# Optimization experiments

Hardware: AMD Instinct MI355X
Metric: run time of the kernel (lower is better)

Reference implementation:

```python
import jax, jax.numpy as jnp
import numpy as np

B, C, H, W = 4, 64, 64, 64


def setup_inputs() -> dict:
    key = jax.random.key(0)
    k1, k2, k3, k4, k5 = jax.random.split(key, 5)
    return {
        "x": jax.random.normal(k1, (B, C, H, W), dtype=jnp.float32),
        "w_qkv": jax.random.normal(k2, (3 * C, C), dtype=jnp.float32) * (1.0 / np.sqrt(C)),
        "b_qkv": jax.random.normal(k3, (3 * C,), dtype=jnp.float32) * 0.02,
        "w_proj": jax.random.normal(k4, (C, C), dtype=jnp.float32) * (1.0 / np.sqrt(C)),
        "b_proj": jax.random.normal(k5, (C,), dtype=jnp.float32) * 0.02,
    }


def reference(x, w_qkv, b_qkv, w_proj, b_proj):
    b, c, h, w = x.shape
    xf = x.reshape(b, c, h * w)                                  # [B, C, N]
    # 1x1 Conv1d == per-position linear over channels
    qkv = jnp.einsum('oc,bcn->bon', w_qkv, xf) + b_qkv[None, :, None]  # [B, 3C, N]
    q, k, v = jnp.split(qkv, 3, axis=1)                          # each [B, C, N]
    scores = jnp.einsum('bcn,bcm->bnm', q, k) / (c ** 0.5)       # [B, N, N]
    attn = jax.nn.softmax(scores, axis=-1)
    out = jnp.einsum('bcm,bnm->bcn', v, attn)                    # [B, C, N]
    out = jnp.einsum('oc,bcn->bon', w_proj, out) + b_proj[None, :, None]
    return out.reshape(b, c, h, w) + x
```

## Files before the change

### kernel.cpp

```cpp
#include <hip/hip_runtime.h>

typedef __bf16 bf16x8 __attribute__((ext_vector_type(8)));
typedef __bf16 bf16x4 __attribute__((ext_vector_type(4)));
typedef __bf16 bf16x2 __attribute__((ext_vector_type(2)));
typedef float f32x4 __attribute__((ext_vector_type(4)));
typedef short s16x4 __attribute__((ext_vector_type(4)));

#define NB 4
#define NC 64
#define NN 4096
#define SPLIT 8

#define QSCALE (0.125f * 1.44269504088896340736f)

#if __has_builtin(__builtin_amdgcn_exp2f)
#define EXP2(x) __builtin_amdgcn_exp2f(x)
#else
#define EXP2(x) exp2f(x)
#endif

__global__ __launch_bounds__(256) void qkv_kernel(
    const float* __restrict__ x, const float* __restrict__ wqkv,
    const float* __restrict__ bqkv,
    __bf16* __restrict__ Qg, __bf16* __restrict__ Kg, __bf16* __restrict__ Vg)
{
  const int tid = threadIdx.x;
  const int b = blockIdx.y;
  const int z = blockIdx.z;
  const int tsel = z >> 3;
  const int obase = (z & 7) * 8;
  const int n = blockIdx.x * 512 + tid * 2;
  const float wscale = (tsel == 0) ? QSCALE : 1.0f;

  __shared__ float wsh[8 * 64];
  __shared__ float bsh[8];
  wsh[tid]       = wqkv[(tsel * 64 + obase) * 64 + tid] * wscale;
  wsh[tid + 256] = wqkv[(tsel * 64 + obase) * 64 + tid + 256] * wscale;
  if (tid < 8) bsh[tid] = bqkv[tsel * 64 + obase + tid] * wscale;
  __syncthreads();

  float xa[64], xb[64];
#pragma unroll
  for (int c = 0; c < 64; c++) {
    const float2 t = *(const float2*)&x[((size_t)(b * 64 + c)) * NN + n];
    xa[c] = t.x; xb[c] = t.y;
  }

  float aa[8], ab[8];
#pragma unroll
  for (int j = 0; j < 8; j++) { aa[j] = bsh[j]; ab[j] = bsh[j]; }
#pragma unroll
  for (int c4 = 0; c4 < 64; c4 += 4) {
#pragma unroll
    for (int j = 0; j < 8; j++) {
      const float4 wv = *(const float4*)&wsh[j * 64 + c4];
      aa[j] = fmaf(wv.x, xa[c4 + 0], aa[j]);
      aa[j] = fmaf(wv.y, xa[c4 + 1], aa[j]);
      aa[j] = fmaf(wv.z, xa[c4 + 2], aa[j]);
      aa[j] = fmaf(wv.w, xa[c4 + 3], aa[j]);
      ab[j] = fmaf(wv.x, xb[c4 + 0], ab[j]);
      ab[j] = fmaf(wv.y, xb[c4 + 1], ab[j]);
      ab[j] = fmaf(wv.z, xb[c4 + 2], ab[j]);
      ab[j] = fmaf(wv.w, xb[c4 + 3], ab[j]);
    }
  }

  if (tsel == 2) {
#pragma unroll
    for (int j = 0; j < 8; j++) {
      bf16x2 pv;
      pv[0] = (__bf16)aa[j]; pv[1] = (__bf16)ab[j];
      *(bf16x2*)(Vg + ((size_t)(b * 64 + obase + j)) * NN + n) = pv;
    }
  } else {
    __bf16* base = (tsel == 0 ? Qg : Kg);
    bf16x8 p0, p1;
#pragma unroll
    for (int j = 0; j < 8; j++) { p0[j] = (__bf16)aa[j]; p1[j] = (__bf16)ab[j]; }
    *(bf16x8*)(base + ((size_t)(b * NN + n)) * 64 + obase) = p0;
    *(bf16x8*)(base + ((size_t)(b * NN + n + 1)) * 64 + obase) = p1;
  }
}

__global__ __launch_bounds__(256) void flash_kernel(
    const __bf16* __restrict__ Q, const __bf16* __restrict__ K,
    const __bf16* __restrict__ V, __bf16* __restrict__ Opart,
    float* __restrict__ lpart)
{
  const int b = blockIdx.y;
  const int s = blockIdx.z;
  const int tid = threadIdx.x;
  const int wave = tid >> 6;
  const int lane = tid & 63;
  const int quad = lane >> 4;
  const int l16 = lane & 15;

  __shared__ __bf16 Kt[64 * 72];
  __shared__ __bf16 Vt[64 * 72];

  const int q0 = blockIdx.x * 128 + wave * 32;

  bf16x8 qf[2][2];
#pragma unroll
  for (int qt = 0; qt < 2; qt++) {
    const __bf16* qrow = Q + ((size_t)(b * NN + q0 + qt * 16 + l16)) * 64;
    qf[qt][0] = *(const bf16x8*)(qrow + quad * 8);
    qf[qt][1] = *(const bf16x8*)(qrow + 32 + quad * 8);
  }

  f32x4 acc[2][4];
#pragma unroll
  for (int qt = 0; qt < 2; qt++)
#pragma unroll
    for (int ct = 0; ct < 4; ct++) acc[qt][ct] = (f32x4){0.f, 0.f, 0.f, 0.f};
  float l[2] = {0.f, 0.f};

  const int kbeg = s * (NN / SPLIT);
  const int kend = kbeg + (NN / SPLIT);
#pragma unroll 1
  for (int kt0 = kbeg; kt0 < kend; kt0 += 64) {
    __syncthreads();
#pragma unroll
    for (int it = 0; it < 2; it++) {
      const int chunk = tid + it * 256;
      const int row = chunk >> 3, col8 = (chunk & 7) * 8;
      *(bf16x8*)(&Kt[row * 72 + col8]) =
          *(const bf16x8*)(K + ((size_t)(b * NN + kt0 + row)) * 64 + col8);
      *(bf16x8*)(&Vt[row * 72 + col8]) =
          *(const bf16x8*)(V + ((size_t)(b * 64 + row)) * NN + kt0 + col8);
    }
    __syncthreads();

    s16x4 pk[4][2];
#pragma unroll
    for (int t = 0; t < 4; t++) {
      const bf16x8 kf0 = *(const bf16x8*)(&Kt[(t * 16 + l16) * 72 + quad * 8]);
      const bf16x8 kf1 = *(const bf16x8*)(&Kt[(t * 16 + l16) * 72 + 32 + quad * 8]);
#pragma unroll
      for (int qt = 0; qt < 2; qt++) {
        f32x4 z = (f32x4){0.f, 0.f, 0.f, 0.f};
        z = __builtin_amdgcn_mfma_f32_16x16x32_bf16(kf0, qf[qt][0], z, 0, 0, 0);
        z = __builtin_amdgcn_mfma_f32_16x16x32_bf16(kf1, qf[qt][1], z, 0, 0, 0);
        const float p0 = EXP2(z[0]), p1 = EXP2(z[1]);
        const float p2 = EXP2(z[2]), p3 = EXP2(z[3]);
        l[qt] += (p0 + p1) + (p2 + p3);
        bf16x4 pv;
        pv[0] = (__bf16)p0; pv[1] = (__bf16)p1;
        pv[2] = (__bf16)p2; pv[3] = (__bf16)p3;
        pk[t][qt] = __builtin_bit_cast(s16x4, pv);
      }
    }

#pragma unroll
    for (int kg = 0; kg < 4; kg++) {
#pragma unroll
      for (int ct = 0; ct < 4; ct++) {
        const bf16x4 va =
            *(const bf16x4*)(&Vt[(ct * 16 + l16) * 72 + kg * 16 + quad * 4]);
        const s16x4 a = __builtin_bit_cast(s16x4, va);
        acc[0][ct] = __builtin_amdgcn_mfma_f32_16x16x16bf16_1k(
            a, pk[kg][0], acc[0][ct], 0, 0, 0);
        acc[1][ct] = __builtin_amdgcn_mfma_f32_16x16x16bf16_1k(
            a, pk[kg][1], acc[1][ct], 0, 0, 0);
      }
    }
  }

#pragma unroll
  for (int qt = 0; qt < 2; qt++) {
    float lr = l[qt];
    lr += __shfl_xor(lr, 16);
    lr += __shfl_xor(lr, 32);
    if (quad == 0)
      lpart[((size_t)(s * NB + b)) * NN + q0 + qt * 16 + l16] = lr;
#pragma unroll
    for (int ct = 0; ct < 4; ct++)
#pragma unroll
      for (int r = 0; r < 4; r++)
        Opart[(((size_t)(s * NB + b)) * 64 + ct * 16 + quad * 4 + r) * NN +
              q0 + qt * 16 + l16] = (__bf16)acc[qt][ct][r];
  }
}

__global__ __launch_bounds__(256) void combine_proj_kernel(
    const __bf16* __restrict__ Opart, const float* __restrict__ lpart,
    const float* __restrict__ wproj, const float* __restrict__ bproj,
    const float* __restrict__ x, float* __restrict__ out)
{
  const int b = blockIdx.y;
  const int n0 = blockIdx.x * 32;
  const int tid = threadIdx.x;

  __shared__ float Ot[64 * 36];
  __shared__ float wT[64 * 66];
  __shared__ float lsh[32];
  __shared__ float bsh[64];

  if (tid < 32) {
    float lt = 0.f;
#pragma unroll
    for (int s = 0; s < SPLIT; s++)
      lt += lpart[((size_t)(s * NB + b)) * NN + n0 + tid];
    lsh[tid] = 1.0f / lt;
  }
  if (tid < 64) bsh[tid] = bproj[tid];
#pragma unroll
  for (int k = 0; k < 16; k++) {
    const int i = tid + k * 256;
    wT[(i & 63) * 66 + (i >> 6)] = wproj[i];
  }
  __syncthreads();

  {
    const int c = tid >> 2;
    const int n8 = (tid & 3) * 8;
    float o[8];
#pragma unroll
    for (int j = 0; j < 8; j++) o[j] = 0.f;
#pragma unroll
    for (int s = 0; s < SPLIT; s++) {
      const bf16x8 v = *(const bf16x8*)(
          Opart + (((size_t)(s * NB + b)) * 64 + c) * NN + n0 + n8);
#pragma unroll
      for (int j = 0; j < 8; j++) o[j] += (float)v[j];
    }
#pragma unroll
    for (int j = 0; j < 8; j++) Ot[c * 36 + n8 + j] = o[j] * lsh[n8 + j];
  }
  __syncthreads();

  const int co = (tid >> 3) * 2;
  const int ng = (tid & 7) * 4;
  float a0[4], a1[4];
#pragma unroll
  for (int j = 0; j < 4; j++) { a0[j] = bsh[co]; a1[j] = bsh[co + 1]; }
  for (int cin = 0; cin < 64; cin++) {
    const float4 ov = *(const float4*)&Ot[cin * 36 + ng];
    const float2 wv = *(const float2*)&wT[cin * 66 + co];
    a0[0] = fmaf(wv.x, ov.x, a0[0]); a0[1] = fmaf(wv.x, ov.y, a0[1]);
    a0[2] = fmaf(wv.x, ov.z, a0[2]); a0[3] = fmaf(wv.x, ov.w, a0[3]);
    a1[0] = fmaf(wv.y, ov.x, a1[0]); a1[1] = fmaf(wv.y, ov.y, a1[1]);
    a1[2] = fmaf(wv.y, ov.z, a1[2]); a1[3] = fmaf(wv.y, ov.w, a1[3]);
  }

#pragma unroll
  for (int i = 0; i < 2; i++) {
    float* ai = (i == 0) ? a0 : a1;
    const size_t base = ((size_t)(b * 64 + co + i)) * NN + n0 + ng;
    const float4 xr = *(const float4*)&x[base];
    float4 r;
    r.x = ai[0] + xr.x; r.y = ai[1] + xr.y;
    r.z = ai[2] + xr.z; r.w = ai[3] + xr.w;
    *(float4*)&out[base] = r;
  }
}

extern "C" void kernel_launch(void* const* d_in, const int* in_sizes, int n_in,
                              void* d_out, int out_size, void* d_ws, size_t ws_size,
                              hipStream_t stream) {
  const float* x     = (const float*)d_in[0];
  const float* wqkv  = (const float*)d_in[1];
  const float* bqkv  = (const float*)d_in[2];
  const float* wproj = (const float*)d_in[3];
  const float* bproj = (const float*)d_in[4];
  float* out = (float*)d_out;

  char* ws = (char*)d_ws;
  __bf16* Q     = (__bf16*)(ws);
  __bf16* K     = (__bf16*)(ws + (2u << 20));
  __bf16* V     = (__bf16*)(ws + (4u << 20));
  __bf16* Opart = (__bf16*)(ws + (6u << 20));
  float*  lpart = (float*)(ws + (23u << 20));

  qkv_kernel<<<dim3(8, NB, 24), 256, 0, stream>>>(x, wqkv, bqkv, Q, K, V);
  flash_kernel<<<dim3(32, NB, SPLIT), 256, 0, stream>>>(Q, K, V, Opart, lpart);
  combine_proj_kernel<<<dim3(128, NB), 256, 0, stream>>>(Opart, lpart, wproj,
                                                         bproj, x, out);
}
```

Before: 113.7 us.

## Fuse output projection into flash kernel via MFMA before split combine

```diff
diff --git a/kernel.cpp b/kernel.cpp
--- a/kernel.cpp
+++ b/kernel.cpp
@@ -84,8 +84,8 @@
 
 __global__ __launch_bounds__(256) void flash_kernel(
     const __bf16* __restrict__ Q, const __bf16* __restrict__ K,
-    const __bf16* __restrict__ V, __bf16* __restrict__ Opart,
-    float* __restrict__ lpart)
+    const __bf16* __restrict__ V, const float* __restrict__ wproj,
+    __bf16* __restrict__ Opart, float* __restrict__ lpart)
 {
   const int b = blockIdx.y;
   const int s = blockIdx.z;
@@ -173,86 +173,90 @@
     lr += __shfl_xor(lr, 32);
     if (quad == 0)
       lpart[((size_t)(s * NB + b)) * NN + q0 + qt * 16 + l16] = lr;
-#pragma unroll
-    for (int ct = 0; ct < 4; ct++)
+  }
+
+  s16x4 ob[2][4];
+#pragma unroll
+  for (int qt = 0; qt < 2; qt++)
+#pragma unroll
+    for (int ch = 0; ch < 4; ch++) {
+      bf16x4 t;
+#pragma unroll
+      for (int r = 0; r < 4; r++) t[r] = (__bf16)acc[qt][ch][r];
+      ob[qt][ch] = __builtin_bit_cast(s16x4, t);
+    }
+
+#pragma unroll
+  for (int cot = 0; cot < 4; cot++) {
+    f32x4 po[2];
+    po[0] = (f32x4){0.f, 0.f, 0.f, 0.f};
+    po[1] = (f32x4){0.f, 0.f, 0.f, 0.f};
+#pragma unroll
+    for (int ch = 0; ch < 4; ch++) {
+      const float4 wv =
+          *(const float4*)&wproj[(cot * 16 + l16) * 64 + ch * 16 + quad * 4];
+      bf16x4 wb;
+      wb[0] = (__bf16)wv.x; wb[1] = (__bf16)wv.y;
+      wb[2] = (__bf16)wv.z; wb[3] = (__bf16)wv.w;
+      const s16x4 a = __builtin_bit_cast(s16x4, wb);
+      po[0] = __builtin_amdgcn_mfma_f32_16x16x16bf16_1k(a, ob[0][ch], po[0], 0, 0, 0);
+      po[1] = __builtin_amdgcn_mfma_f32_16x16x16bf16_1k(a, ob[1][ch], po[1], 0, 0, 0);
+    }
+#pragma unroll
+    for (int qt = 0; qt < 2; qt++)
 #pragma unroll
       for (int r = 0; r < 4; r++)
-        Opart[(((size_t)(s * NB + b)) * 64 + ct * 16 + quad * 4 + r) * NN +
-              q0 + qt * 16 + l16] = (__bf16)acc[qt][ct][r];
-  }
-}
-
-__global__ __launch_bounds__(256) void combine_proj_kernel(
+        Opart[(((size_t)(s * NB + b)) * 64 + cot * 16 + quad * 4 + r) * NN +
+              q0 + qt * 16 + l16] = (__bf16)po[qt][r];
+  }
+}
+
+__global__ __launch_bounds__(256) void combine_kernel(
     const __bf16* __restrict__ Opart, const float* __restrict__ lpart,
-    const float* __restrict__ wproj, const float* __restrict__ bproj,
-    const float* __restrict__ x, float* __restrict__ out)
+    const float* __restrict__ bproj, const float* __restrict__ x,
+    float* __restrict__ out)
 {
   const int b = blockIdx.y;
   const int n0 = blockIdx.x * 32;
   const int tid = threadIdx.x;
 
-  __shared__ float Ot[64 * 36];
-  __shared__ float wT[64 * 66];
-  __shared__ float lsh[32];
-  __shared__ float bsh[64];
-
+  __shared__ float linv[32];
   if (tid < 32) {
     float lt = 0.f;
 #pragma unroll
     for (int s = 0; s < SPLIT; s++)
       lt += lpart[((size_t)(s * NB + b)) * NN + n0 + tid];
-    lsh[tid] = 1.0f / lt;
-  }
-  if (tid < 64) bsh[tid] = bproj[tid];
-#pragma unroll
-  for (int k = 0; k < 16; k++) {
-    const int i = tid + k * 256;
-    wT[(i & 63) * 66 + (i >> 6)] = wproj[i];
+    linv[tid] = 1.0f / lt;
   }
   __syncthreads();
 
-  {
-    const int c = tid >> 2;
-    const int n8 = (tid & 3) * 8;
-    float o[8];
-#pragma unroll
-    for (int j = 0; j < 8; j++) o[j] = 0.f;
-#pragma unroll
-    for (int s = 0; s < SPLIT; s++) {
-      const bf16x8 v = *(const bf16x8*)(
-          Opart + (((size_t)(s * NB + b)) * 64 + c) * NN + n0 + n8);
-#pragma unroll
-      for (int j = 0; j < 8; j++) o[j] += (float)v[j];
-    }
-#pragma unroll
-    for (int j = 0; j < 8; j++) Ot[c * 36 + n8 + j] = o[j] * lsh[n8 + j];
-  }
-  __syncthreads();
-
-  const int co = (tid >> 3) * 2;
-  const int ng = (tid & 7) * 4;
-  float a0[4], a1[4];
-#pragma unroll
-  for (int j = 0; j < 4; j++) { a0[j] = bsh[co]; a1[j] = bsh[co + 1]; }
-  for (int cin = 0; cin < 64; cin++) {
-    const float4 ov = *(const float4*)&Ot[cin * 36 + ng];
-    const float2 wv = *(const float2*)&wT[cin * 66 + co];
-    a0[0] = fmaf(wv.x, ov.x, a0[0]); a0[1] = fmaf(wv.x, ov.y, a0[1]);
-    a0[2] = fmaf(wv.x, ov.z, a0[2]); a0[3] = fmaf(wv.x, ov.w, a0[3]);
-    a1[0] = fmaf(wv.y, ov.x, a1[0]); a1[1] = fmaf(wv.y, ov.y, a1[1]);
-    a1[2] = fmaf(wv.y, ov.z, a1[2]); a1[3] = fmaf(wv.y, ov.w, a1[3]);
-  }
-
-#pragma unroll
-  for (int i = 0; i < 2; i++) {
-    float* ai = (i == 0) ? a0 : a1;
-    const size_t base = ((size_t)(b * 64 + co + i)) * NN + n0 + ng;
-    const float4 xr = *(const float4*)&x[base];
-    float4 r;
-    r.x = ai[0] + xr.x; r.y = ai[1] + xr.y;
-    r.z = ai[2] + xr.z; r.w = ai[3] + xr.w;
-    *(float4*)&out[base] = r;
-  }
+  const int c = tid >> 2;
+  const int n8 = (tid & 3) * 8;
+
+  float o[8];
+#pragma unroll
+  for (int j = 0; j < 8; j++) o[j] = 0.f;
+#pragma unroll
+  for (int s = 0; s < SPLIT; s++) {
+    const bf16x8 v = *(const bf16x8*)(
+        Opart + (((size_t)(s * NB + b)) * 64 + c) * NN + n0 + n8);
+#pragma unroll
+    for (int j = 0; j < 8; j++) o[j] += (float)v[j];
+  }
+
+  const float bb = bproj[c];
+  const float4 li0 = *(const float4*)&linv[n8];
+  const float4 li1 = *(const float4*)&linv[n8 + 4];
+  const size_t base = ((size_t)(b * 64 + c)) * NN + n0 + n8;
+  const float4 x0 = *(const float4*)&x[base];
+  const float4 x1 = *(const float4*)&x[base + 4];
+  float4 r0, r1;
+  r0.x = o[0] * li0.x + bb + x0.x;  r0.y = o[1] * li0.y + bb + x0.y;
+  r0.z = o[2] * li0.z + bb + x0.z;  r0.w = o[3] * li0.w + bb + x0.w;
+  r1.x = o[4] * li1.x + bb + x1.x;  r1.y = o[5] * li1.y + bb + x1.y;
+  r1.z = o[6] * li1.z + bb + x1.z;  r1.w = o[7] * li1.w + bb + x1.w;
+  *(float4*)&out[base] = r0;
+  *(float4*)&out[base + 4] = r1;
 }
 
 extern "C" void kernel_launch(void* const* d_in, const int* in_sizes, int n_in,
@@ -273,7 +277,8 @@
   float*  lpart = (float*)(ws + (23u << 20));
 
   qkv_kernel<<<dim3(8, NB, 24), 256, 0, stream>>>(x, wqkv, bqkv, Q, K, V);
-  flash_kernel<<<dim3(32, NB, SPLIT), 256, 0, stream>>>(Q, K, V, Opart, lpart);
-  combine_proj_kernel<<<dim3(128, NB), 256, 0, stream>>>(Opart, lpart, wproj,
-                                                         bproj, x, out);
-}
+  flash_kernel<<<dim3(32, NB, SPLIT), 256, 0, stream>>>(Q, K, V, wproj,
+                                                        Opart, lpart);
+  combine_kernel<<<dim3(128, NB), 256, 0, stream>>>(Opart, lpart, bproj, x,
+                                                    out);
+}
```

After: 115.1 us. No clear change (+1.2%).
